# Performance work log

Measured on AMD Instinct MI355X. Metric: run time of the kernel, lower is better.

The kernel has to match this reference:

```python
import jax, jax.numpy as jnp
import numpy as np

HID = 128


def setup_inputs() -> dict:
    key = jax.random.key(0)
    ks = jax.random.split(key, 7)
    B = 131072
    X = jax.random.normal(ks[0], (B, 4), dtype=jnp.float32)
    # Linear params stored as (in, out); scaled ~ 1/sqrt(fan_in) like torch default
    W1 = jax.random.normal(ks[1], (4, HID), dtype=jnp.float32) * 0.5
    b1 = jnp.zeros((HID,), jnp.float32)
    W2 = jax.random.normal(ks[2], (HID, HID), dtype=jnp.float32) * (1.0 / np.sqrt(HID))
    b2 = jnp.zeros((HID,), jnp.float32)
    W3 = jax.random.normal(ks[3], (HID, 1), dtype=jnp.float32) * (1.0 / np.sqrt(HID))
    b3 = jnp.zeros((1,), jnp.float32)
    return {"X": X, "W1": W1, "b1": b1, "W2": W2, "b2": b2, "W3": W3, "b3": b3}


def reference(X, W1, b1, W2, b2, W3, b3):
    def V_fn(feat):  # feat: [4] -> scalar potential
        h = jnp.tanh(feat @ W1 + b1)
        h = jnp.tanh(h @ W2 + b2)
        return (h @ W3 + b3)[0]

    def L_single(q, qd):  # q:[2], qd:[2] -> scalar Lagrangian
        t1, t2 = q[0], q[1]
        w1, w2 = qd[0], qd[1]
        T = w1 ** 2 + 0.5 * w2 ** 2 + w1 * w2 * jnp.cos(t1 - t2)
        feat = jnp.stack([jnp.sin(t1), jnp.cos(t1), jnp.sin(t2), jnp.cos(t2)])
        return T - V_fn(feat)

    q = X[:, :2]
    qd = X[:, 2:]
    dL_dq = jax.vmap(jax.grad(L_single, argnums=0))(q, qd)          # [B,2]
    # mass matrix M[i,j] = d^2 L / (d qd_i d qd_j)
    M = jax.vmap(jax.jacfwd(jax.grad(L_single, argnums=1), argnums=1))(q, qd)  # [B,2,2]
    # cross Hessian H[i,j] = d^2 L / (d qd_i d q_j); Coriolis C_i = H[i,:] @ qd
    H = jax.vmap(jax.jacfwd(jax.grad(L_single, argnums=1), argnums=0))(q, qd)  # [B,2,2]
    C = jnp.einsum('bij,bj->bi', H, qd)                              # [B,2]
    qdd = jnp.linalg.solve(M, (dL_dq - C)[..., None])[..., 0]        # [B,2]
    return jnp.concatenate([qd, qdd], axis=1)                        # [B,4]
```

## Files before the change

kernel.cpp:

```cpp
#include <hip/hip_runtime.h>
#include <math.h>

#define HID 128
#define TPB 1024
#define NW  16
#define GRIDB 256

typedef __bf16 bf16;
typedef bf16 bf16x8 __attribute__((ext_vector_type(8)));
typedef bf16 bf16x4 __attribute__((ext_vector_type(4)));
typedef float floatx4 __attribute__((ext_vector_type(4)));

__device__ __forceinline__ floatx4 tanh4(floatx4 z) {
    floatx4 t = z * 2.885390081777927f;
    floatx4 e = { __builtin_amdgcn_exp2f(t[0]), __builtin_amdgcn_exp2f(t[1]),
                  __builtin_amdgcn_exp2f(t[2]), __builtin_amdgcn_exp2f(t[3]) };
    e = e + 1.0f;
    floatx4 r = { __builtin_amdgcn_rcpf(e[0]), __builtin_amdgcn_rcpf(e[1]),
                  __builtin_amdgcn_rcpf(e[2]), __builtin_amdgcn_rcpf(e[3]) };
    return 1.0f - 2.0f * r;
}


__global__ __launch_bounds__(TPB, 1)
void lnn_kernel(const float* __restrict__ X,
                const float* __restrict__ W1,
                const float* __restrict__ b1,
                const float* __restrict__ b2,
                const float* __restrict__ W3,
                const float* __restrict__ W2,
                float* __restrict__ out,
                int B, int nchunk)
{
    __shared__ __align__(16) bf16 sW2A[16384];
    __shared__ __align__(16) bf16 sW2R[16384];
    __shared__ __align__(16) bf16 sXf[NW][2048];
    __shared__ __align__(16) bf16 sW1A[4][512];
    __shared__ __align__(16) float sW1r[4][HID];
    __shared__ __align__(16) float sB1[HID], sB2[HID], sW3[HID];

    const int tid  = threadIdx.x;
    const int w    = tid >> 6;
    const int lane = tid & 63;
    const int lrow = lane & 15;
    const int lq   = lane >> 4;
    const int swz  = lrow & 3;

    if (tid < 512) { int r = tid >> 7, j = tid & (HID - 1); sW1r[r][j] = W1[r * HID + j]; }
    if (tid < HID) sB1[tid] = b1[tid];
    else if (tid < 2 * HID) sB2[tid - HID] = b2[tid - HID];
    else if (tid < 3 * HID) sW3[tid - 2 * HID] = W3[tid - 2 * HID];

    #pragma unroll
    for (int tt = 0; tt < 2; ++tt) {
        int e = tid + tt * TPB;
        int t = e >> 6, l = e & 63;
        int a = t >> 2, bidx = t & 3;
        int lr = l & 15, q = l >> 4;
        bf16x8 f;
        #pragma unroll
        for (int idx = 0; idx < 8; ++idx)
            f[idx] = (bf16)W2[(32*bidx + 8*q + idx) * HID + 16*a + lr];
        *reinterpret_cast<bf16x8*>(&sW2A[e * 8]) = f;
        const float4* rp = reinterpret_cast<const float4*>(&W2[(16*a + lr) * HID + 32*bidx + 8*q]);
        float4 r0 = rp[0], r1 = rp[1];
        bf16x8 g;
        g[0]=(bf16)r0.x; g[1]=(bf16)r0.y; g[2]=(bf16)r0.z; g[3]=(bf16)r0.w;
        g[4]=(bf16)r1.x; g[5]=(bf16)r1.y; g[6]=(bf16)r1.z; g[7]=(bf16)r1.w;
        *reinterpret_cast<bf16x8*>(&sW2R[e * 8]) = g;
    }
    if (tid < 256) {
        int m = tid >> 6, l = tid & 63;
        int lr = l & 15, q = l >> 4;
        bf16x8 f = {};
        if (lr < 4) {
            #pragma unroll
            for (int idx = 0; idx < 8; ++idx)
                f[idx] = (bf16)W1[lr * HID + 32*m + 8*q + idx];
        }
        *reinterpret_cast<bf16x8*>(&sW1A[m][l * 8]) = f;
    }
    __syncthreads();

    bf16* const myX = &sXf[w][0];

    const int tileStride = GRIDB * NW;
    const int t0 = (int)blockIdx.x * NW + w;
    const floatx4 fz = floatx4{0.f,0.f,0.f,0.f};

    auto loadX = [&](int t) -> float4 {
        int gc = t * 16 + lrow; gc = gc < B ? gc : (B - 1);
        return reinterpret_cast<const float4*>(X)[gc];
    };

    float4 xc = loadX(t0);

    #pragma unroll 1
    for (int c = 0; c < nchunk; ++c) {
        const int tile = t0 + c * tileStride;
        if (tile * 16 >= B) break;
        const int S0 = tile * 16;
        float4 xn = loadX(tile + tileStride);

        float s1, c1, s2, c2;
        __sincosf(xc.x, &s1, &c1);
        __sincosf(xc.y, &s2, &c2);
        const float qd1 = xc.z, qd2 = xc.w;

        bf16x8 breg[4];
        #pragma unroll
        for (int kt = 0; kt < 4; ++kt) {
            int jb = 32 * kt + 8 * lq;
            floatx4 w0a = *reinterpret_cast<const floatx4*>(&sW1r[0][jb]);
            floatx4 w0b = *reinterpret_cast<const floatx4*>(&sW1r[0][jb+4]);
            floatx4 w1a = *reinterpret_cast<const floatx4*>(&sW1r[1][jb]);
            floatx4 w1b = *reinterpret_cast<const floatx4*>(&sW1r[1][jb+4]);
            floatx4 w2a = *reinterpret_cast<const floatx4*>(&sW1r[2][jb]);
            floatx4 w2b = *reinterpret_cast<const floatx4*>(&sW1r[2][jb+4]);
            floatx4 w3a = *reinterpret_cast<const floatx4*>(&sW1r[3][jb]);
            floatx4 w3b = *reinterpret_cast<const floatx4*>(&sW1r[3][jb+4]);
            floatx4 bba = *reinterpret_cast<const floatx4*>(&sB1[jb]);
            floatx4 bbb = *reinterpret_cast<const floatx4*>(&sB1[jb+4]);
            floatx4 za = bba + s1*w0a + c1*w1a + s2*w2a + c2*w3a;
            floatx4 zb = bbb + s1*w0b + c1*w1b + s2*w2b + c2*w3b;
            floatx4 ha = tanh4(za);
            floatx4 hb = tanh4(zb);
            bf16x8 hf;
            hf[0]=(bf16)ha[0]; hf[1]=(bf16)ha[1]; hf[2]=(bf16)ha[2]; hf[3]=(bf16)ha[3];
            hf[4]=(bf16)hb[0]; hf[5]=(bf16)hb[1]; hf[6]=(bf16)hb[2]; hf[7]=(bf16)hb[3];
            breg[kt] = hf;
        }

        #pragma unroll
        for (int jt = 0; jt < 8; ++jt) {
            floatx4 acc = __builtin_amdgcn_mfma_f32_16x16x32_bf16(
                *reinterpret_cast<const bf16x8*>(&sW2A[((jt*4 + 0)*64 + lane)*8]),
                breg[0], fz, 0,0,0);
            #pragma unroll
            for (int kt = 1; kt < 4; ++kt)
                acc = __builtin_amdgcn_mfma_f32_16x16x32_bf16(
                    *reinterpret_cast<const bf16x8*>(&sW2A[((jt*4 + kt)*64 + lane)*8]),
                    breg[kt], acc, 0,0,0);
            int jb = 16*jt + 4*lq;
            floatx4 b2v = *reinterpret_cast<const floatx4*>(&sB2[jb]);
            floatx4 w3v = *reinterpret_cast<const floatx4*>(&sW3[jb]);
            floatx4 h = tanh4(acc + b2v);
            floatx4 gv = (1.0f - h*h) * w3v;
            bf16x4 g;
            g[0]=(bf16)gv[0]; g[1]=(bf16)gv[1]; g[2]=(bf16)gv[2]; g[3]=(bf16)gv[3];
            int blk = (2*(jt&1) + (lq>>1)) ^ swz;
            *reinterpret_cast<bf16x4*>(&myX[(jt>>1)*512 + lrow*32 + blk*8 + 4*(lq&1)]) = g;
        }

        bf16x8 gB[4];
        #pragma unroll
        for (int L = 0; L < 4; ++L)
            gB[L] = *reinterpret_cast<const bf16x8*>(&myX[L*512 + lrow*32 + (lq ^ swz)*8]);

        #pragma unroll
        for (int it = 0; it < 8; ++it) {
            floatx4 acc2 = __builtin_amdgcn_mfma_f32_16x16x32_bf16(
                *reinterpret_cast<const bf16x8*>(&sW2R[((it*4 + 0)*64 + lane)*8]),
                gB[0], fz, 0,0,0);
            #pragma unroll
            for (int jt2 = 1; jt2 < 4; ++jt2)
                acc2 = __builtin_amdgcn_mfma_f32_16x16x32_bf16(
                    *reinterpret_cast<const bf16x8*>(&sW2R[((it*4 + jt2)*64 + lane)*8]),
                    gB[jt2], acc2, 0,0,0);
            bf16x4 g;
            g[0]=(bf16)acc2[0]; g[1]=(bf16)acc2[1];
            g[2]=(bf16)acc2[2]; g[3]=(bf16)acc2[3];
            int blk = (2*(it&1) + (lq>>1)) ^ swz;
            *reinterpret_cast<bf16x4*>(&myX[(it>>1)*512 + lrow*32 + blk*8 + 4*(lq&1)]) = g;
        }

        floatx4 dv = fz;
        #pragma unroll
        for (int m = 0; m < 4; ++m) {
            bf16x8 sv = *reinterpret_cast<const bf16x8*>(&myX[m*512 + lrow*32 + (lq ^ swz)*8]);
            bf16x8 g1;
            #pragma unroll
            for (int idx = 0; idx < 8; ++idx) {
                float h = (float)breg[m][idx];
                float s = (float)sv[idx];
                g1[idx] = (bf16)(s - s*h*h);
            }
            dv = __builtin_amdgcn_mfma_f32_16x16x32_bf16(
                *reinterpret_cast<const bf16x8*>(&sW1A[m][lane*8]), g1, dv, 0,0,0);
        }

        if (lane < 16 && S0 + lane < B) {
            float dV0 = dv[0], dV1 = dv[1], dV2 = dv[2], dV3 = dv[3];
            float cosD = c1 * c2 + s1 * s2;
            float sinD = s1 * c2 - c1 * s2;
            float dVt1 = dV0 * c1 - dV1 * s1;
            float dVt2 = dV2 * c2 - dV3 * s2;
            float sT = qd1 * qd2 * sinD;
            float cw = sinD * (qd2 - qd1);
            float rhs1 = (-sT - dVt1) - qd2 * cw;
            float rhs2 = ( sT - dVt2) - qd1 * cw;
            float det = 2.0f - cosD * cosD;
            float inv = __builtin_amdgcn_rcpf(det);
            float qdd1 = (rhs1 - cosD * rhs2) * inv;
            float qdd2 = (2.0f * rhs2 - cosD * rhs1) * inv;
            *reinterpret_cast<float4*>(&out[4 * (S0 + lane)]) = make_float4(qd1, qd2, qdd1, qdd2);
        }
        xc = xn;
    }
}

extern "C" void kernel_launch(void* const* d_in, const int* in_sizes, int n_in,
                              void* d_out, int out_size, void* d_ws, size_t ws_size,
                              hipStream_t stream) {
    const float* X  = (const float*)d_in[0];
    const float* W1 = (const float*)d_in[1];
    const float* b1 = (const float*)d_in[2];
    const float* W2 = (const float*)d_in[3];
    const float* b2 = (const float*)d_in[4];
    const float* W3 = (const float*)d_in[5];
    float* out = (float*)d_out;
    int B = in_sizes[0] / 4;
    int tiles = (B + 15) >> 4;
    int nchunk = (tiles + GRIDB * NW - 1) / (GRIDB * NW);
    lnn_kernel<<<GRIDB, TPB, 0, stream>>>(X, W1, b1, b2, W3, W2, out, B, nchunk);
}
```

Before: 91.54 us.

## Process two 16-sample tiles per wave sharing each W2 fragment load

Each wave now handles two 16-row tiles per iteration, so every W2 A-fragment read from LDS feeds two independent MFMA chains. The per-wave LDS scratch shrinks to two 512-element buffers that are reused block by block instead of one full 2048-element buffer. The prefetch of the next X tile is dropped. The aim is to halve LDS weight traffic per sample and to interleave independent MFMA chains for better latency hiding, at the cost of more registers and half as many loop iterations to spread across waves.

```diff
diff --git a/kernel.cpp b/kernel.cpp
--- a/kernel.cpp
+++ b/kernel.cpp
@@ -34,7 +34,7 @@
 {
     __shared__ __align__(16) bf16 sW2A[16384];
     __shared__ __align__(16) bf16 sW2R[16384];
-    __shared__ __align__(16) bf16 sXf[NW][2048];
+    __shared__ __align__(16) bf16 sXf[NW][1024];
     __shared__ __align__(16) bf16 sW1A[4][512];
     __shared__ __align__(16) float sW1r[4][HID];
     __shared__ __align__(16) float sB1[HID], sB2[HID], sW3[HID];
@@ -82,32 +82,30 @@
     }
     __syncthreads();
 
-    bf16* const myX = &sXf[w][0];
-
-    const int tileStride = GRIDB * NW;
-    const int t0 = (int)blockIdx.x * NW + w;
+    bf16* const lb0 = &sXf[w][0];
+    bf16* const lb1 = &sXf[w][512];
+
+    const int dualStride = GRIDB * NW;
+    const int d0 = (int)blockIdx.x * NW + w;
     const floatx4 fz = floatx4{0.f,0.f,0.f,0.f};
-
-    auto loadX = [&](int t) -> float4 {
-        int gc = t * 16 + lrow; gc = gc < B ? gc : (B - 1);
-        return reinterpret_cast<const float4*>(X)[gc];
-    };
-
-    float4 xc = loadX(t0);
 
     #pragma unroll 1
     for (int c = 0; c < nchunk; ++c) {
-        const int tile = t0 + c * tileStride;
-        if (tile * 16 >= B) break;
-        const int S0 = tile * 16;
-        float4 xn = loadX(tile + tileStride);
-
-        float s1, c1, s2, c2;
-        __sincosf(xc.x, &s1, &c1);
-        __sincosf(xc.y, &s2, &c2);
-        const float qd1 = xc.z, qd2 = xc.w;
-
-        bf16x8 breg[4];
+        const int dt = d0 + c * dualStride;
+        const int S0 = dt * 32;
+        if (S0 >= B) break;
+
+        int ga = S0 + lrow;      ga = ga < B ? ga : (B - 1);
+        int gb = S0 + 16 + lrow; gb = gb < B ? gb : (B - 1);
+        float4 x0 = reinterpret_cast<const float4*>(X)[ga];
+        float4 x1 = reinterpret_cast<const float4*>(X)[gb];
+        float s1a, c1a, s2a, c2a, s1b, c1b, s2b, c2b;
+        __sincosf(x0.x, &s1a, &c1a);
+        __sincosf(x0.y, &s2a, &c2a);
+        __sincosf(x1.x, &s1b, &c1b);
+        __sincosf(x1.y, &s2b, &c2b);
+
+        bf16x8 breg0[4], breg1[4];
         #pragma unroll
         for (int kt = 0; kt < 4; ++kt) {
             int jb = 32 * kt + 8 * lq;
@@ -121,80 +119,100 @@
             floatx4 w3b = *reinterpret_cast<const floatx4*>(&sW1r[3][jb+4]);
             floatx4 bba = *reinterpret_cast<const floatx4*>(&sB1[jb]);
             floatx4 bbb = *reinterpret_cast<const floatx4*>(&sB1[jb+4]);
-            floatx4 za = bba + s1*w0a + c1*w1a + s2*w2a + c2*w3a;
-            floatx4 zb = bbb + s1*w0b + c1*w1b + s2*w2b + c2*w3b;
-            floatx4 ha = tanh4(za);
-            floatx4 hb = tanh4(zb);
+            floatx4 za = bba + s1a*w0a + c1a*w1a + s2a*w2a + c2a*w3a;
+            floatx4 zb = bbb + s1a*w0b + c1a*w1b + s2a*w2b + c2a*w3b;
+            floatx4 ha = tanh4(za), hb = tanh4(zb);
             bf16x8 hf;
             hf[0]=(bf16)ha[0]; hf[1]=(bf16)ha[1]; hf[2]=(bf16)ha[2]; hf[3]=(bf16)ha[3];
             hf[4]=(bf16)hb[0]; hf[5]=(bf16)hb[1]; hf[6]=(bf16)hb[2]; hf[7]=(bf16)hb[3];
-            breg[kt] = hf;
-        }
-
-        #pragma unroll
-        for (int jt = 0; jt < 8; ++jt) {
-            floatx4 acc = __builtin_amdgcn_mfma_f32_16x16x32_bf16(
-                *reinterpret_cast<const bf16x8*>(&sW2A[((jt*4 + 0)*64 + lane)*8]),
-                breg[0], fz, 0,0,0);
-            #pragma unroll
-            for (int kt = 1; kt < 4; ++kt)
-                acc = __builtin_amdgcn_mfma_f32_16x16x32_bf16(
-                    *reinterpret_cast<const bf16x8*>(&sW2A[((jt*4 + kt)*64 + lane)*8]),
-                    breg[kt], acc, 0,0,0);
-            int jb = 16*jt + 4*lq;
-            floatx4 b2v = *reinterpret_cast<const floatx4*>(&sB2[jb]);
-            floatx4 w3v = *reinterpret_cast<const floatx4*>(&sW3[jb]);
-            floatx4 h = tanh4(acc + b2v);
-            floatx4 gv = (1.0f - h*h) * w3v;
-            bf16x4 g;
-            g[0]=(bf16)gv[0]; g[1]=(bf16)gv[1]; g[2]=(bf16)gv[2]; g[3]=(bf16)gv[3];
-            int blk = (2*(jt&1) + (lq>>1)) ^ swz;
-            *reinterpret_cast<bf16x4*>(&myX[(jt>>1)*512 + lrow*32 + blk*8 + 4*(lq&1)]) = g;
-        }
-
-        bf16x8 gB[4];
-        #pragma unroll
-        for (int L = 0; L < 4; ++L)
-            gB[L] = *reinterpret_cast<const bf16x8*>(&myX[L*512 + lrow*32 + (lq ^ swz)*8]);
-
-        #pragma unroll
-        for (int it = 0; it < 8; ++it) {
-            floatx4 acc2 = __builtin_amdgcn_mfma_f32_16x16x32_bf16(
-                *reinterpret_cast<const bf16x8*>(&sW2R[((it*4 + 0)*64 + lane)*8]),
-                gB[0], fz, 0,0,0);
-            #pragma unroll
-            for (int jt2 = 1; jt2 < 4; ++jt2)
-                acc2 = __builtin_amdgcn_mfma_f32_16x16x32_bf16(
-                    *reinterpret_cast<const bf16x8*>(&sW2R[((it*4 + jt2)*64 + lane)*8]),
-                    gB[jt2], acc2, 0,0,0);
-            bf16x4 g;
-            g[0]=(bf16)acc2[0]; g[1]=(bf16)acc2[1];
-            g[2]=(bf16)acc2[2]; g[3]=(bf16)acc2[3];
-            int blk = (2*(it&1) + (lq>>1)) ^ swz;
-            *reinterpret_cast<bf16x4*>(&myX[(it>>1)*512 + lrow*32 + blk*8 + 4*(lq&1)]) = g;
-        }
-
-        floatx4 dv = fz;
-        #pragma unroll
-        for (int m = 0; m < 4; ++m) {
-            bf16x8 sv = *reinterpret_cast<const bf16x8*>(&myX[m*512 + lrow*32 + (lq ^ swz)*8]);
-            bf16x8 g1;
+            breg0[kt] = hf;
+            za = bba + s1b*w0a + c1b*w1a + s2b*w2a + c2b*w3a;
+            zb = bbb + s1b*w0b + c1b*w1b + s2b*w2b + c2b*w3b;
+            ha = tanh4(za); hb = tanh4(zb);
+            hf[0]=(bf16)ha[0]; hf[1]=(bf16)ha[1]; hf[2]=(bf16)ha[2]; hf[3]=(bf16)ha[3];
+            hf[4]=(bf16)hb[0]; hf[5]=(bf16)hb[1]; hf[6]=(bf16)hb[2]; hf[7]=(bf16)hb[3];
+            breg1[kt] = hf;
+        }
+
+        bf16x8 gB0[4], gB1[4];
+        #pragma unroll
+        for (int L = 0; L < 4; ++L) {
+            #pragma unroll
+            for (int b = 0; b < 2; ++b) {
+                int jt = 2*L + b;
+                bf16x8 A = *reinterpret_cast<const bf16x8*>(&sW2A[((jt*4 + 0)*64 + lane)*8]);
+                floatx4 a0 = __builtin_amdgcn_mfma_f32_16x16x32_bf16(A, breg0[0], fz, 0,0,0);
+                floatx4 a1 = __builtin_amdgcn_mfma_f32_16x16x32_bf16(A, breg1[0], fz, 0,0,0);
+                #pragma unroll
+                for (int kt = 1; kt < 4; ++kt) {
+                    A = *reinterpret_cast<const bf16x8*>(&sW2A[((jt*4 + kt)*64 + lane)*8]);
+                    a0 = __builtin_amdgcn_mfma_f32_16x16x32_bf16(A, breg0[kt], a0, 0,0,0);
+                    a1 = __builtin_amdgcn_mfma_f32_16x16x32_bf16(A, breg1[kt], a1, 0,0,0);
+                }
+                int jb = 16*jt + 4*lq;
+                floatx4 b2v = *reinterpret_cast<const floatx4*>(&sB2[jb]);
+                floatx4 w3v = *reinterpret_cast<const floatx4*>(&sW3[jb]);
+                int blk = (2*b + (lq>>1)) ^ swz;
+                int eoff = lrow*32 + blk*8 + 4*(lq&1);
+                floatx4 h = tanh4(a0 + b2v);
+                floatx4 gv = (1.0f - h*h) * w3v;
+                bf16x4 g;
+                g[0]=(bf16)gv[0]; g[1]=(bf16)gv[1]; g[2]=(bf16)gv[2]; g[3]=(bf16)gv[3];
+                *reinterpret_cast<bf16x4*>(&lb0[eoff]) = g;
+                h = tanh4(a1 + b2v);
+                gv = (1.0f - h*h) * w3v;
+                g[0]=(bf16)gv[0]; g[1]=(bf16)gv[1]; g[2]=(bf16)gv[2]; g[3]=(bf16)gv[3];
+                *reinterpret_cast<bf16x4*>(&lb1[eoff]) = g;
+            }
+            gB0[L] = *reinterpret_cast<const bf16x8*>(&lb0[lrow*32 + (lq ^ swz)*8]);
+            gB1[L] = *reinterpret_cast<const bf16x8*>(&lb1[lrow*32 + (lq ^ swz)*8]);
+        }
+
+        floatx4 dv0 = fz, dv1 = fz;
+        #pragma unroll
+        for (int L = 0; L < 4; ++L) {
+            #pragma unroll
+            for (int b = 0; b < 2; ++b) {
+                int it = 2*L + b;
+                bf16x8 A = *reinterpret_cast<const bf16x8*>(&sW2R[((it*4 + 0)*64 + lane)*8]);
+                floatx4 a0 = __builtin_amdgcn_mfma_f32_16x16x32_bf16(A, gB0[0], fz, 0,0,0);
+                floatx4 a1 = __builtin_amdgcn_mfma_f32_16x16x32_bf16(A, gB1[0], fz, 0,0,0);
+                #pragma unroll
+                for (int jt2 = 1; jt2 < 4; ++jt2) {
+                    A = *reinterpret_cast<const bf16x8*>(&sW2R[((it*4 + jt2)*64 + lane)*8]);
+                    a0 = __builtin_amdgcn_mfma_f32_16x16x32_bf16(A, gB0[jt2], a0, 0,0,0);
+                    a1 = __builtin_amdgcn_mfma_f32_16x16x32_bf16(A, gB1[jt2], a1, 0,0,0);
+                }
+                int blk = (2*b + (lq>>1)) ^ swz;
+                int eoff = lrow*32 + blk*8 + 4*(lq&1);
+                bf16x4 g;
+                g[0]=(bf16)a0[0]; g[1]=(bf16)a0[1]; g[2]=(bf16)a0[2]; g[3]=(bf16)a0[3];
+                *reinterpret_cast<bf16x4*>(&lb0[eoff]) = g;
+                g[0]=(bf16)a1[0]; g[1]=(bf16)a1[1]; g[2]=(bf16)a1[2]; g[3]=(bf16)a1[3];
+                *reinterpret_cast<bf16x4*>(&lb1[eoff]) = g;
+            }
+            bf16x8 sv0 = *reinterpret_cast<const bf16x8*>(&lb0[lrow*32 + (lq ^ swz)*8]);
+            bf16x8 sv1 = *reinterpret_cast<const bf16x8*>(&lb1[lrow*32 + (lq ^ swz)*8]);
+            bf16x8 A3 = *reinterpret_cast<const bf16x8*>(&sW1A[L][lane*8]);
+            bf16x8 g10, g11;
             #pragma unroll
             for (int idx = 0; idx < 8; ++idx) {
-                float h = (float)breg[m][idx];
-                float s = (float)sv[idx];
-                g1[idx] = (bf16)(s - s*h*h);
+                float h0 = (float)breg0[L][idx], s0v = (float)sv0[idx];
+                float h1 = (float)breg1[L][idx], s1v = (float)sv1[idx];
+                g10[idx] = (bf16)(s0v - s0v*h0*h0);
+                g11[idx] = (bf16)(s1v - s1v*h1*h1);
             }
-            dv = __builtin_amdgcn_mfma_f32_16x16x32_bf16(
-                *reinterpret_cast<const bf16x8*>(&sW1A[m][lane*8]), g1, dv, 0,0,0);
+            dv0 = __builtin_amdgcn_mfma_f32_16x16x32_bf16(A3, g10, dv0, 0,0,0);
+            dv1 = __builtin_amdgcn_mfma_f32_16x16x32_bf16(A3, g11, dv1, 0,0,0);
         }
 
         if (lane < 16 && S0 + lane < B) {
-            float dV0 = dv[0], dV1 = dv[1], dV2 = dv[2], dV3 = dv[3];
-            float cosD = c1 * c2 + s1 * s2;
-            float sinD = s1 * c2 - c1 * s2;
-            float dVt1 = dV0 * c1 - dV1 * s1;
-            float dVt2 = dV2 * c2 - dV3 * s2;
+            float dV0 = dv0[0], dV1 = dv0[1], dV2 = dv0[2], dV3 = dv0[3];
+            float cosD = c1a * c2a + s1a * s2a;
+            float sinD = s1a * c2a - c1a * s2a;
+            float dVt1 = dV0 * c1a - dV1 * s1a;
+            float dVt2 = dV2 * c2a - dV3 * s2a;
+            float qd1 = x0.z, qd2 = x0.w;
             float sT = qd1 * qd2 * sinD;
             float cw = sinD * (qd2 - qd1);
             float rhs1 = (-sT - dVt1) - qd2 * cw;
@@ -205,7 +223,23 @@
             float qdd2 = (2.0f * rhs2 - cosD * rhs1) * inv;
             *reinterpret_cast<float4*>(&out[4 * (S0 + lane)]) = make_float4(qd1, qd2, qdd1, qdd2);
         }
-        xc = xn;
+        if (lane < 16 && S0 + 16 + lane < B) {
+            float dV0 = dv1[0], dV1 = dv1[1], dV2 = dv1[2], dV3 = dv1[3];
+            float cosD = c1b * c2b + s1b * s2b;
+            float sinD = s1b * c2b - c1b * s2b;
+            float dVt1 = dV0 * c1b - dV1 * s1b;
+            float dVt2 = dV2 * c2b - dV3 * s2b;
+            float qd1 = x1.z, qd2 = x1.w;
+            float sT = qd1 * qd2 * sinD;
+            float cw = sinD * (qd2 - qd1);
+            float rhs1 = (-sT - dVt1) - qd2 * cw;
+            float rhs2 = ( sT - dVt2) - qd1 * cw;
+            float det = 2.0f - cosD * cosD;
+            float inv = __builtin_amdgcn_rcpf(det);
+            float qdd1 = (rhs1 - cosD * rhs2) * inv;
+            float qdd2 = (2.0f * rhs2 - cosD * rhs1) * inv;
+            *reinterpret_cast<float4*>(&out[4 * (S0 + 16 + lane)]) = make_float4(qd1, qd2, qdd1, qdd2);
+        }
     }
 }
 
@@ -220,7 +254,7 @@
     const float* W3 = (const float*)d_in[5];
     float* out = (float*)d_out;
     int B = in_sizes[0] / 4;
-    int tiles = (B + 15) >> 4;
-    int nchunk = (tiles + GRIDB * NW - 1) / (GRIDB * NW);
+    int duals = (B + 31) >> 5;
+    int nchunk = (duals + GRIDB * NW - 1) / (GRIDB * NW);
     lnn_kernel<<<GRIDB, TPB, 0, stream>>>(X, W1, b1, b2, W3, W2, out, B, nchunk);
 }
```

New measurement: 99.59 us. +8.8%, slower.
